# Performance work log

Hardware: AMD Instinct MI355X
Metric: run time of the kernel (lower is better)

The kernel has to match this reference:

```python
import jax, jax.numpy as jnp
import numpy as np


def setup_inputs() -> dict:
    key = jax.random.key(0)
    ks = jax.random.split(key, 11)
    B, S, D, K = 8, 2048, 512, 256
    s = lambda k, shp, fan: jax.random.normal(k, shp, dtype=jnp.float32) / np.sqrt(fan)
    return {
        "x": jax.random.normal(ks[0], (B, S, D), dtype=jnp.float32),
        "Wk1": s(ks[1], (D, K), D), "bk1": jnp.zeros((K,), jnp.float32),
        "Wq1": s(ks[2], (D, K), D), "bq1": jnp.zeros((K,), jnp.float32),
        "Wk2": s(ks[3], (D, K), D), "bk2": jnp.zeros((K,), jnp.float32),
        "Wq2": s(ks[4], (D, K), D), "bq2": jnp.zeros((K,), jnp.float32),
        "Wv2": s(ks[5], (D, D), D), "bv2": jnp.zeros((D,), jnp.float32),
    }


def _attn(q, k, v):
    # raw scores with NO 1/sqrt(d) scaling, softmax over key axis, then AV
    scores = jax.nn.softmax(jnp.einsum('bqd,bkd->bqk', q, k), axis=-1)
    return jnp.einsum('bqk,bkd->bqd', scores, v)


def _block2(h, Wk2, bk2, Wq2, bq2, Wv2, bv2):
    k = h @ Wk2 + bk2
    q = h @ Wq2 + bq2
    v = h @ Wv2 + bv2
    v = v / jnp.linalg.norm(v, axis=2, keepdims=True)  # L2-normalize values
    return _attn(q, k, v)


def reference(x, Wk1, bk1, Wq1, bq1, Wk2, bk2, Wq2, bq2, Wv2, bv2):
    # block 1: values are the raw input x
    k1 = x @ Wk1 + bk1
    q1 = x @ Wq1 + bq1
    outputs = _attn(q1, k1, x)
    # blocks 2 and 3 reuse the SAME layer-2 weights (as in the torch forward)
    hidden = _block2(outputs, Wk2, bk2, Wq2, bq2, Wv2, bv2)
    final = _block2(hidden, Wk2, bk2, Wq2, bq2, Wv2, bv2)
    return final[0, -1, :]
```

## Files before the change

### kernel.cpp

```cpp
#include <hip/hip_runtime.h>
#include <math.h>

typedef __attribute__((ext_vector_type(8))) short short8;
typedef __attribute__((ext_vector_type(4))) float f32x4;
typedef unsigned short us;

__device__ inline unsigned short f2bf_rn(float f) {
    unsigned u = __builtin_bit_cast(unsigned, f);
    u += 0x7FFF + ((u >> 16) & 1);
    return (unsigned short)(u >> 16);
}
__device__ inline float bf2f(unsigned short h) {
    unsigned u = ((unsigned)h) << 16;
    return __builtin_bit_cast(float, u);
}

#define ISSUE(ST, RA, RB)                                                      \
  do {                                                                         \
    int s_ = (ST);                                                             \
    int sg_ = s_ / SPS;                                                        \
    int k0_ = (s_ - sg_ * SPS) * 64;                                           \
    const unsigned short* Ap_ = (sg_ < 2) ? Ah : Al;                           \
    const unsigned short* Bp_ = (sg_ == 1) ? Bl : Bh;                          \
    _Pragma("unroll") for (int i_ = 0; i_ < 4; ++i_) {                         \
      RA[i_] = *(const uint4*)(Ap_ + (size_t)(bm + crow[i_]) * lda + k0_ + csl[i_] * 8); \
      RB[i_] = *(const uint4*)(Bp_ + (size_t)(bn + crow[i_]) * ldb + k0_ + csl[i_] * 8); \
    }                                                                          \
  } while (0)

#define PHASE(IT, RWa, RWb, RLa, RLb)                                          \
  do {                                                                         \
    _Pragma("unroll") for (int i_ = 0; i_ < 4; ++i_) {                         \
      int wsl_ = csl[i_] ^ (crow[i_] & 7);                                     \
      *(uint4*)&As[crow[i_]][wsl_ * 8] = RWa[i_];                              \
      *(uint4*)&Bs[crow[i_]][wsl_ * 8] = RWb[i_];                              \
    }                                                                          \
    if ((IT) + 1 < CHUNK) { ISSUE(st0 + (IT) + 1, RLa, RLb); }                 \
    asm volatile("s_waitcnt lgkmcnt(0)\n\ts_barrier" ::: "memory");            \
    _Pragma("unroll") for (int kk = 0; kk < 2; ++kk) {                         \
      short8 af[4], bf[4];                                                     \
      _Pragma("unroll") for (int f = 0; f < 4; ++f) {                          \
        int ar = wm * 64 + f * 16 + r15;                                       \
        int as_ = (kk * 4 + ksl) ^ (ar & 7);                                   \
        af[f] = *(const short8*)&As[ar][as_ * 8];                              \
        int br = wn * 64 + f * 16 + r15;                                       \
        int bs_ = (kk * 4 + ksl) ^ (br & 7);                                   \
        bf[f] = *(const short8*)&Bs[br][bs_ * 8];                              \
      }                                                                        \
      _Pragma("unroll") for (int i_ = 0; i_ < 4; ++i_)                         \
        _Pragma("unroll") for (int j_ = 0; j_ < 4; ++j_)                       \
          acc[i_][j_] = __builtin_amdgcn_mfma_f32_16x16x32_bf16(               \
              af[i_], bf[j_], acc[i_][j_], 0, 0, 0);                           \
    }                                                                          \
    asm volatile("s_barrier" ::: "memory");                                    \
  } while (0)

template <int KSEG, int NSPLIT>
__global__ __launch_bounds__(256, 2) void gemm_bf16(
    const unsigned short* __restrict__ Ah, const unsigned short* __restrict__ Al, int lda,
    const unsigned short* __restrict__ Bh, const unsigned short* __restrict__ Bl, int ldb,
    float* __restrict__ Cout, int ldc)
{
    constexpr int SPS = KSEG / 64;
    constexpr int NST = 3 * SPS;
    constexpr int CHUNK = NST / NSPLIT;

    __shared__ __align__(16) unsigned short As[128][64];
    __shared__ __align__(16) unsigned short Bs[128][64];

    const int tid = threadIdx.x, lane = tid & 63, w = tid >> 6;
    const int wm = w >> 1, wn = w & 1;
    const int bm = blockIdx.y * 128, bn = blockIdx.x * 128;
    const int st0 = blockIdx.z * CHUNK;
    const int r15 = lane & 15, ksl = lane >> 4;

    int crow[4], csl[4];
#pragma unroll
    for (int i = 0; i < 4; ++i) { int c = tid + i * 256; crow[i] = c >> 3; csl[i] = c & 7; }

    f32x4 acc[4][4];
#pragma unroll
    for (int i = 0; i < 4; ++i)
#pragma unroll
        for (int j = 0; j < 4; ++j) acc[i][j] = (f32x4){0.f, 0.f, 0.f, 0.f};

    uint4 rA0[4], rB0[4], rA1[4], rB1[4];
    ISSUE(st0, rA0, rB0);

#pragma unroll 1
    for (int it = 0; it < CHUNK; it += 2) {
        PHASE(it,     rA0, rB0, rA1, rB1);
        PHASE(it + 1, rA1, rB1, rA0, rB0);
    }

    float* Cz = Cout + (size_t)blockIdx.z * (size_t)(gridDim.y * 128) * ldc;
#pragma unroll
    for (int i = 0; i < 4; ++i) {
        int rowb = bm + wm * 64 + i * 16 + (lane >> 4) * 4;
#pragma unroll
        for (int j = 0; j < 4; ++j) {
            int colb = bn + wn * 64 + j * 16 + r15;
#pragma unroll
            for (int r = 0; r < 4; ++r)
                Cz[(size_t)(rowb + r) * ldc + colb] = acc[i][j][r];
        }
    }
}

template <int NS, bool BIAS, bool L2N>
__global__ __launch_bounds__(256) void reduce_kernel(
    const float* __restrict__ part, size_t pstride4,
    const float* __restrict__ bias, float* __restrict__ C,
    unsigned short* __restrict__ Ch, unsigned short* __restrict__ Cl, int N)
{
    __shared__ float red[4];
    const int tid = threadIdx.x;
    size_t idx = (size_t)blockIdx.x * 256 + tid;
    const float4* p = (const float4*)part;
    float4 s = p[idx];
#pragma unroll
    for (int z = 1; z < NS; ++z) {
        float4 t = p[idx + (size_t)z * pstride4];
        s.x += t.x; s.y += t.y; s.z += t.z; s.w += t.w;
    }
    if (BIAS) {
        int col = (int)((idx * 4) & (size_t)(N - 1));
        s.x += bias[col]; s.y += bias[col + 1]; s.z += bias[col + 2]; s.w += bias[col + 3];
    }
    if (L2N) {
        float ss = (tid >= 128) ? (s.x * s.x + s.y * s.y + s.z * s.z + s.w * s.w) : 0.f;
#pragma unroll
        for (int o = 32; o; o >>= 1) ss += __shfl_down(ss, o);
        if ((tid & 63) == 0) red[tid >> 6] = ss;
        __syncthreads();
        if (tid >= 128) {
            float scale = 1.f / sqrtf(red[2] + red[3]);
            s.x *= scale; s.y *= scale; s.z *= scale; s.w *= scale;
        }
    }
    ((float4*)C)[idx] = s;
    float v[4] = {s.x, s.y, s.z, s.w};
    unsigned short h[4], l[4];
#pragma unroll
    for (int q = 0; q < 4; ++q) { h[q] = f2bf_rn(v[q]); l[q] = f2bf_rn(v[q] - bf2f(h[q])); }
    uint2 hp = make_uint2((unsigned)h[0] | ((unsigned)h[1] << 16), (unsigned)h[2] | ((unsigned)h[3] << 16));
    uint2 lp = make_uint2((unsigned)l[0] | ((unsigned)l[1] << 16), (unsigned)l[2] | ((unsigned)l[3] << 16));
    ((uint2*)Ch)[idx] = hp;
    ((uint2*)Cl)[idx] = lp;
}

#define SLK(r, s) ((s) ^ (((s) >> 3) & 3) ^ ((((r) ^ ((r) >> 3))) & 7))

__global__ __launch_bounds__(256, 2) void flash_attn(
    const unsigned short* __restrict__ Qh, const unsigned short* __restrict__ Ql,
    const unsigned short* __restrict__ Kh, const unsigned short* __restrict__ Kl,
    int ldqk,
    const unsigned short* __restrict__ VTh, const unsigned short* __restrict__ VTl,
    float* __restrict__ Opart, float* __restrict__ Mpart, float* __restrict__ Lpart)
{
    const int tid = threadIdx.x, lane = tid & 63, w = tid >> 6;
    const int z = blockIdx.x;
    const int q0 = blockIdx.y * 64;
    const int dblk = blockIdx.z;
    const int s0 = z * 256;
    const int cc = lane & 15, g = lane >> 4;
    const int dbase = dblk * 256 + w * 64;

    __shared__ __align__(16) unsigned short KsH[32][256], KsL[32][256];
    __shared__ __align__(16) unsigned short PsH[64][32], PsL[64][32];
    __shared__ float Fs[64];
    __shared__ int flagAny[4];

    short8 qh[8], qlv[8];
#pragma unroll
    for (int ks = 0; ks < 8; ++ks) {
        const size_t qoff = (size_t)(q0 + w * 16 + cc) * ldqk + ks * 32 + g * 8;
        qh[ks]  = *(const short8*)(Qh + qoff);
        qlv[ks] = *(const short8*)(Ql + qoff);
    }

    f32x4 acc[4][4];
#pragma unroll
    for (int a = 0; a < 4; ++a)
#pragma unroll
        for (int b = 0; b < 4; ++b) acc[a][b] = (f32x4){0.f, 0.f, 0.f, 0.f};
    float m[4] = {-1e30f, -1e30f, -1e30f, -1e30f};
    float l[4] = {0.f, 0.f, 0.f, 0.f};

#pragma unroll 1
    for (int sub = 0; sub < 8; ++sub) {
        __syncthreads();
#pragma unroll
        for (int i = 0; i < 4; ++i) {
            int idx = tid + i * 256;
            int row = (idx >> 3) & 31;
            int sl  = (idx & 7) | ((idx >> 8) << 3);
            size_t go = (size_t)(s0 + sub * 32 + row) * ldqk + sl * 8;
            uint4 vh = *(const uint4*)(Kh + go);
            uint4 vl = *(const uint4*)(Kl + go);
            int sw = SLK(row, sl);
            *(uint4*)&KsH[row][sw * 8] = vh;
            *(uint4*)&KsL[row][sw * 8] = vl;
        }
        __syncthreads();

        f32x4 sac[2];
        sac[0] = (f32x4){0.f, 0.f, 0.f, 0.f};
        sac[1] = (f32x4){0.f, 0.f, 0.f, 0.f};
#pragma unroll
        for (int ks = 0; ks < 8; ++ks) {
#pragma unroll
            for (int t = 0; t < 2; ++t) {
                int row = t * 16 + cc;
                int sw = SLK(row, ks * 4 + g);
                short8 bh = *(const short8*)&KsH[row][sw * 8];
                short8 bl = *(const short8*)&KsL[row][sw * 8];
                sac[t] = __builtin_amdgcn_mfma_f32_16x16x32_bf16(qh[ks], bh, sac[t], 0, 0, 0);
                sac[t] = __builtin_amdgcn_mfma_f32_16x16x32_bf16(qh[ks], bl, sac[t], 0, 0, 0);
                sac[t] = __builtin_amdgcn_mfma_f32_16x16x32_bf16(qlv[ks], bh, sac[t], 0, 0, 0);
            }
        }

        float mt[4], fr[4];
        bool nb = false;
#pragma unroll
        for (int r = 0; r < 4; ++r) {
            float v = fmaxf(sac[0][r], sac[1][r]);
#pragma unroll
            for (int o = 8; o >= 1; o >>= 1) v = fmaxf(v, __shfl_xor(v, o));
            mt[r] = v;
            nb = nb || (v > m[r] + 8.f);
        }
        const int need = __any((int)nb);
        if (need) {
#pragma unroll
            for (int r = 0; r < 4; ++r) {
                float mn = fmaxf(m[r], mt[r]);
                fr[r] = __expf(m[r] - mn);
                m[r] = mn;
                l[r] *= fr[r];
            }
        } else {
#pragma unroll
            for (int r = 0; r < 4; ++r) fr[r] = 1.f;
        }
        if (cc == 0) {
#pragma unroll
            for (int r = 0; r < 4; ++r) Fs[w * 16 + g * 4 + r] = fr[r];
        }
        if (lane == 0) flagAny[w] = need;

#pragma unroll
        for (int t = 0; t < 2; ++t) {
            float ps[4];
#pragma unroll
            for (int r = 0; r < 4; ++r) {
                float pv = __expf(sac[t][r] - m[r]);
                ps[r] = pv;
                unsigned short ph = f2bf_rn(pv);
                unsigned short pl = f2bf_rn(pv - bf2f(ph));
                int qq = w * 16 + g * 4 + r;
                int kv = cc + 16 * t;
                int col = (((kv >> 3) ^ (qq & 3)) << 3) | (kv & 7);
                PsH[qq][col] = ph;
                PsL[qq][col] = pl;
            }
#pragma unroll
            for (int r = 0; r < 4; ++r) {
                float sv = ps[r];
#pragma unroll
                for (int o = 8; o >= 1; o >>= 1) sv += __shfl_xor(sv, o);
                l[r] += sv;
            }
        }
        __syncthreads();

        int anyf = flagAny[0] | flagAny[1] | flagAny[2] | flagAny[3];
        if (anyf) {
#pragma unroll
            for (int qt = 0; qt < 4; ++qt)
#pragma unroll
                for (int r = 0; r < 4; ++r) {
                    float fq = Fs[qt * 16 + g * 4 + r];
#pragma unroll
                    for (int dt = 0; dt < 4; ++dt) acc[qt][dt][r] *= fq;
                }
        }

        short8 pah[4], pal[4];
#pragma unroll
        for (int qt = 0; qt < 4; ++qt) {
            int qr = qt * 16 + cc;
            int col = (g ^ (qr & 3)) << 3;
            pah[qt] = *(const short8*)&PsH[qr][col];
            pal[qt] = *(const short8*)&PsL[qr][col];
        }
#pragma unroll
        for (int dt = 0; dt < 4; ++dt) {
            size_t vo = (size_t)(dbase + dt * 16 + cc) * 2048 + s0 + sub * 32 + g * 8;
            short8 vh = *(const short8*)(VTh + vo);
            short8 vl = *(const short8*)(VTl + vo);
#pragma unroll
            for (int qt = 0; qt < 4; ++qt) {
                acc[qt][dt] = __builtin_amdgcn_mfma_f32_16x16x32_bf16(pah[qt], vh, acc[qt][dt], 0, 0, 0);
                acc[qt][dt] = __builtin_amdgcn_mfma_f32_16x16x32_bf16(pah[qt], vl, acc[qt][dt], 0, 0, 0);
                acc[qt][dt] = __builtin_amdgcn_mfma_f32_16x16x32_bf16(pal[qt], vh, acc[qt][dt], 0, 0, 0);
            }
        }
    }

#pragma unroll
    for (int qt = 0; qt < 4; ++qt)
#pragma unroll
        for (int dt = 0; dt < 4; ++dt)
#pragma unroll
            for (int r = 0; r < 4; ++r) {
                int row = q0 + qt * 16 + g * 4 + r;
                int col = dbase + dt * 16 + cc;
                Opart[((size_t)z * 2048 + row) * 512 + col] = acc[qt][dt][r];
            }
    if (dblk == 0 && cc == 0) {
#pragma unroll
        for (int r = 0; r < 4; ++r) {
            int row = q0 + w * 16 + g * 4 + r;
            Mpart[z * 2048 + row] = m[r];
            Lpart[z * 2048 + row] = l[r];
        }
    }
}

__global__ __launch_bounds__(256) void flash_combine(
    const float* __restrict__ Opart, const float* __restrict__ Mpart,
    const float* __restrict__ Lpart,
    unsigned short* __restrict__ Oh, unsigned short* __restrict__ Ol)
{
    const int q = blockIdx.x;
    const int tid = threadIdx.x;
    float wz[8];
    float mstar = -1e30f;
#pragma unroll
    for (int zz = 0; zz < 8; ++zz) { wz[zz] = Mpart[zz * 2048 + q]; mstar = fmaxf(mstar, wz[zz]); }
    float L = 0.f;
#pragma unroll
    for (int zz = 0; zz < 8; ++zz) {
        float e = __expf(wz[zz] - mstar);
        L += e * Lpart[zz * 2048 + q];
        wz[zz] = e;
    }
    float invL = 1.f / L;
    int d = tid * 2;
    float sx = 0.f, sy = 0.f;
#pragma unroll
    for (int zz = 0; zz < 8; ++zz) {
        const float2 t = *(const float2*)(Opart + ((size_t)zz * 2048 + q) * 512 + d);
        sx += wz[zz] * t.x;
        sy += wz[zz] * t.y;
    }
    sx *= invL; sy *= invL;
    unsigned short h0 = f2bf_rn(sx), h1 = f2bf_rn(sy);
    unsigned short l0 = f2bf_rn(sx - bf2f(h0)), l1 = f2bf_rn(sy - bf2f(h1));
    *(unsigned*)(Oh + (size_t)q * 512 + d) = (unsigned)h0 | ((unsigned)h1 << 16);
    *(unsigned*)(Ol + (size_t)q * 512 + d) = (unsigned)l0 | ((unsigned)l1 << 16);
}

__global__ __launch_bounds__(256) void tc_kernel(
    const float* __restrict__ in, int ldin,
    unsigned short* __restrict__ oh, unsigned short* __restrict__ ol,
    int ldo, int rowoff)
{
    __shared__ float tile[32][33];
    int bx = blockIdx.x * 32, by = blockIdx.y * 32;
    int tx = threadIdx.x & 31, ty = threadIdx.x >> 5;
#pragma unroll
    for (int i = 0; i < 32; i += 8)
        tile[ty + i][tx] = in[(size_t)(by + ty + i) * ldin + bx + tx];
    __syncthreads();
#pragma unroll
    for (int i = 0; i < 32; i += 8) {
        float v = tile[tx][ty + i];
        unsigned short h = f2bf_rn(v);
        unsigned short l = f2bf_rn(v - bf2f(h));
        size_t o = (size_t)(rowoff + bx + ty + i) * ldo + by + tx;
        oh[o] = h; ol[o] = l;
    }
}

__global__ __launch_bounds__(256) void convert_hl(
    const float* __restrict__ in, unsigned short* __restrict__ oh,
    unsigned short* __restrict__ ol)
{
    size_t idx = (size_t)blockIdx.x * 256 + threadIdx.x;
    float4 s = ((const float4*)in)[idx];
    float v[4] = {s.x, s.y, s.z, s.w};
    unsigned short h[4], l[4];
#pragma unroll
    for (int q = 0; q < 4; ++q) { h[q] = f2bf_rn(v[q]); l[q] = f2bf_rn(v[q] - bf2f(h[q])); }
    uint2 hp = make_uint2((unsigned)h[0] | ((unsigned)h[1] << 16), (unsigned)h[2] | ((unsigned)h[3] << 16));
    uint2 lp = make_uint2((unsigned)l[0] | ((unsigned)l[1] << 16), (unsigned)l[2] | ((unsigned)l[3] << 16));
    ((uint2*)oh)[idx] = hp;
    ((uint2*)ol)[idx] = lp;
}

__global__ __launch_bounds__(256) void concat_bias(
    const float* bk1, const float* bq1, const float* bk2, const float* bq2,
    const float* bv2, float* b1, float* b2)
{
    int i = blockIdx.x * 256 + threadIdx.x;
    if (i < 512) b1[i] = (i < 256) ? bk1[i] : bq1[i - 256];
    if (i < 1024) b2[i] = (i < 256) ? bk2[i] : (i < 512 ? bq2[i - 256] : bv2[i - 512]);
}

template <bool HAS_BIAS>
__global__ __launch_bounds__(256) void gemv_nt(
    const float* __restrict__ a, const float* __restrict__ Bt, int ldb,
    const float* __restrict__ bias, float* __restrict__ out, int K)
{
    int w = threadIdx.x >> 6, lane = threadIdx.x & 63;
    int n = blockIdx.x * 4 + w;
    const float* row = Bt + (size_t)n * ldb;
    float s = 0.f;
    for (int k = lane; k < K; k += 64) s = fmaf(a[k], row[k], s);
#pragma unroll
    for (int o = 32; o; o >>= 1) s += __shfl_down(s, o);
    if (lane == 0) out[n] = HAS_BIAS ? s + bias[n] : s;
}

__global__ __launch_bounds__(256) void gemv_hl(
    const float* __restrict__ p, const unsigned short* __restrict__ Vh,
    const unsigned short* __restrict__ Vl, int ld, float* __restrict__ out, int K)
{
    int w = threadIdx.x >> 6, lane = threadIdx.x & 63;
    int d = blockIdx.x * 4 + w;
    const unsigned short* rh = Vh + (size_t)d * ld;
    const unsigned short* rl = Vl + (size_t)d * ld;
    float s = 0.f;
    for (int k = lane; k < K; k += 64) s = fmaf(p[k], bf2f(rh[k]) + bf2f(rl[k]), s);
#pragma unroll
    for (int o = 32; o; o >>= 1) s += __shfl_down(s, o);
    if (lane == 0) out[d] = s;
}

__global__ __launch_bounds__(256) void softmax_f32(float* __restrict__ S, int L)
{
    __shared__ float row[2048];
    __shared__ float red[8];
    const int tid = threadIdx.x;
    float* p = S + (size_t)blockIdx.x * L;
    float mx = -1e30f;
    for (int i = tid; i < L; i += 256) { float v = p[i]; row[i] = v; mx = fmaxf(mx, v); }
#pragma unroll
    for (int o = 32; o; o >>= 1) mx = fmaxf(mx, __shfl_down(mx, o));
    if ((tid & 63) == 0) red[tid >> 6] = mx;
    __syncthreads();
    mx = fmaxf(fmaxf(red[0], red[1]), fmaxf(red[2], red[3]));
    float sum = 0.f;
    for (int i = tid; i < L; i += 256) { float e = expf(row[i] - mx); row[i] = e; sum += e; }
#pragma unroll
    for (int o = 32; o; o >>= 1) sum += __shfl_down(sum, o);
    __syncthreads();
    if ((tid & 63) == 0) red[4 + (tid >> 6)] = sum;
    __syncthreads();
    float inv = 1.f / (red[4] + red[5] + red[6] + red[7]);
    for (int i = tid; i < L; i += 256) p[i] = row[i] * inv;
}

extern "C" void kernel_launch(void* const* d_in, const int* in_sizes, int n_in,
                              void* d_out, int out_size, void* d_ws, size_t ws_size,
                              hipStream_t stream)
{
    const float* x   = (const float*)d_in[0];
    const float* Wk1 = (const float*)d_in[1];
    const float* bk1 = (const float*)d_in[2];
    const float* Wq1 = (const float*)d_in[3];
    const float* bq1 = (const float*)d_in[4];
    const float* Wk2 = (const float*)d_in[5];
    const float* bk2 = (const float*)d_in[6];
    const float* Wq2 = (const float*)d_in[7];
    const float* bq2 = (const float*)d_in[8];
    const float* Wv2 = (const float*)d_in[9];
    const float* bv2 = (const float*)d_in[10];
    float* out = (float*)d_out;

    const int S = 2048, D = 512;

    char* p = (char*)d_ws;
    float* C   = (float*)p;  p += (size_t)S * 1024 * 4;
    float* BIG = (float*)p;  p += (size_t)8 * S * 512 * 4;
    float* Mp  = (float*)p;  p += (size_t)8 * S * 4;
    float* Lp  = (float*)p;  p += (size_t)8 * S * 4;
    us* Chh = (us*)p; p += (size_t)S * 1024 * 2;
    us* Cll = (us*)p; p += (size_t)S * 1024 * 2;
    us* Hh  = (us*)p; p += (size_t)S * D * 2;
    us* Hl  = (us*)p; p += (size_t)S * D * 2;
    us* xh  = (us*)p; p += (size_t)S * D * 2;
    us* xl  = (us*)p; p += (size_t)S * D * 2;
    us* VTh = (us*)p; p += (size_t)D * S * 2;
    us* VTl = (us*)p; p += (size_t)D * S * 2;
    us* WT1h = (us*)p; p += (size_t)512 * 512 * 2;
    us* WT1l = (us*)p; p += (size_t)512 * 512 * 2;
    us* WT2h = (us*)p; p += (size_t)1024 * 512 * 2;
    us* WT2l = (us*)p; p += (size_t)1024 * 512 * 2;
    float* b1 = (float*)p; p += 512 * 4;
    float* b2 = (float*)p; p += 1024 * 4;

    dim3 blk(256);
    const size_t PSTR  = (size_t)S * 512 / 4;
    const size_t PSTR2 = (size_t)S * 1024 / 4;

    convert_hl<<<dim3(S * D / 1024), blk, 0, stream>>>(x, xh, xl);
    tc_kernel<<<dim3(16, 64), blk, 0, stream>>>(x, 512, VTh, VTl, S, 0);
    tc_kernel<<<dim3(8, 16), blk, 0, stream>>>(Wk1, 256, WT1h, WT1l, 512, 0);
    tc_kernel<<<dim3(8, 16), blk, 0, stream>>>(Wq1, 256, WT1h, WT1l, 512, 256);
    tc_kernel<<<dim3(8, 16), blk, 0, stream>>>(Wk2, 256, WT2h, WT2l, 512, 0);
    tc_kernel<<<dim3(8, 16), blk, 0, stream>>>(Wq2, 256, WT2h, WT2l, 512, 256);
    tc_kernel<<<dim3(16, 16), blk, 0, stream>>>(Wv2, 512, WT2h, WT2l, 512, 512);
    concat_bias<<<dim3(4), blk, 0, stream>>>(bk1, bq1, bk2, bq2, bv2, b1, b2);

    gemm_bf16<512, 6><<<dim3(4, 16, 6), blk, 0, stream>>>(xh, xl, 512, WT1h, WT1l, 512, BIG, 512);
    reduce_kernel<6, true, false><<<dim3(S * 512 / 1024), blk, 0, stream>>>(BIG, PSTR, b1, C, Chh, Cll, 512);
    flash_attn<<<dim3(8, 32, 2), blk, 0, stream>>>(Chh + 256, Cll + 256, Chh, Cll, 512,
                                                   VTh, VTl, BIG, Mp, Lp);
    flash_combine<<<dim3(S), blk, 0, stream>>>(BIG, Mp, Lp, Hh, Hl);

    gemm_bf16<512, 4><<<dim3(8, 16, 4), blk, 0, stream>>>(Hh, Hl, 512, WT2h, WT2l, 512, BIG, 1024);
    reduce_kernel<4, true, true><<<dim3(S * 1024 / 1024), blk, 0, stream>>>(BIG, PSTR2, b2, C, Chh, Cll, 1024);
    tc_kernel<<<dim3(16, 64), blk, 0, stream>>>(C + 512, 1024, VTh, VTl, S, 0);
    flash_attn<<<dim3(8, 32, 2), blk, 0, stream>>>(Chh + 256, Cll + 256, Chh, Cll, 1024,
                                                   VTh, VTl, BIG, Mp, Lp);
    flash_combine<<<dim3(S), blk, 0, stream>>>(BIG, Mp, Lp, Hh, Hl);

    gemm_bf16<512, 4><<<dim3(8, 16, 4), blk, 0, stream>>>(Hh, Hl, 512, WT2h, WT2l, 512, BIG, 1024);
    reduce_kernel<4, true, true><<<dim3(S * 1024 / 1024), blk, 0, stream>>>(BIG, PSTR2, b2, C, Chh, Cll, 1024);
    tc_kernel<<<dim3(16, 64), blk, 0, stream>>>(C + 512, 1024, VTh, VTl, S, 0);
    gemv_nt<false><<<dim3(S / 4), blk, 0, stream>>>(C + (size_t)(S - 1) * 1024 + 256, C, 1024,
                                                    nullptr, BIG, 256);
    softmax_f32<<<dim3(1), blk, 0, stream>>>(BIG, S);
    gemv_hl<<<dim3(D / 4), blk, 0, stream>>>(BIG, VTh, VTl, S, out, S);
}
```

Before: 389.5 us.

## Prefetch K tiles and V fragments in flash_attn; merge setup kernels

In flash_attn, the K tile for the next sub-block is loaded into registers while the current one is written to shared memory, and the V fragments are issued before the score computation. This hides global load latency behind MFMA work and drops one barrier per iteration. Separately, the eight small setup launches (conversion, transposes, bias concat) are merged into two kernels to cut launch overhead. The trade-off is higher register pressure from the prefetch buffers, which could reduce occupancy at launch_bounds(256,2).

After: 520.5 us. 1.34x slower.

```diff
diff --git a/kernel.cpp b/kernel.cpp
--- a/kernel.cpp
+++ b/kernel.cpp
@@ -64,6 +64,7 @@
     constexpr int SPS = KSEG / 64;
     constexpr int NST = 3 * SPS;
     constexpr int CHUNK = NST / NSPLIT;
+    static_assert((CHUNK & 1) == 0, "CHUNK must be even");
 
     __shared__ __align__(16) unsigned short As[128][64];
     __shared__ __align__(16) unsigned short Bs[128][64];
@@ -150,6 +151,16 @@
 }
 
 #define SLK(r, s) ((s) ^ (((s) >> 3) & 3) ^ ((((r) ^ ((r) >> 3))) & 7))
+
+#define KISSUE(SUB)                                                            \
+  do {                                                                         \
+    int ns_ = (SUB) & 7;                                                       \
+    _Pragma("unroll") for (int i_ = 0; i_ < 4; ++i_) {                         \
+      size_t go_ = (size_t)(s0 + ns_ * 32 + srow[i_]) * ldqk + ssl[i_] * 8;    \
+      krh[i_] = *(const uint4*)(Kh + go_);                                     \
+      krl[i_] = *(const uint4*)(Kl + go_);                                     \
+    }                                                                          \
+  } while (0)
 
 __global__ __launch_bounds__(256, 2) void flash_attn(
     const unsigned short* __restrict__ Qh, const unsigned short* __restrict__ Ql,
@@ -171,6 +182,15 @@
     __shared__ float Fs[64];
     __shared__ int flagAny[4];
 
+    int srow[4], ssl[4], ssw[4];
+#pragma unroll
+    for (int i = 0; i < 4; ++i) {
+        int idx = tid + i * 256;
+        srow[i] = (idx >> 3) & 31;
+        ssl[i]  = (idx & 7) | ((idx >> 8) << 3);
+        ssw[i]  = SLK(srow[i], ssl[i]);
+    }
+
     short8 qh[8], qlv[8];
 #pragma unroll
     for (int ks = 0; ks < 8; ++ks) {
@@ -187,20 +207,24 @@
     float m[4] = {-1e30f, -1e30f, -1e30f, -1e30f};
     float l[4] = {0.f, 0.f, 0.f, 0.f};
 
+    uint4 krh[4], krl[4];
+    KISSUE(0);
+
 #pragma unroll 1
     for (int sub = 0; sub < 8; ++sub) {
-        __syncthreads();
 #pragma unroll
         for (int i = 0; i < 4; ++i) {
-            int idx = tid + i * 256;
-            int row = (idx >> 3) & 31;
-            int sl  = (idx & 7) | ((idx >> 8) << 3);
-            size_t go = (size_t)(s0 + sub * 32 + row) * ldqk + sl * 8;
-            uint4 vh = *(const uint4*)(Kh + go);
-            uint4 vl = *(const uint4*)(Kl + go);
-            int sw = SLK(row, sl);
-            *(uint4*)&KsH[row][sw * 8] = vh;
-            *(uint4*)&KsL[row][sw * 8] = vl;
+            *(uint4*)&KsH[srow[i]][ssw[i] * 8] = krh[i];
+            *(uint4*)&KsL[srow[i]][ssw[i] * 8] = krl[i];
+        }
+        KISSUE(sub + 1);
+
+        uint4 vph[4], vpl[4];
+#pragma unroll
+        for (int dt = 0; dt < 4; ++dt) {
+            size_t vo = (size_t)(dbase + dt * 16 + cc) * 2048 + s0 + sub * 32 + g * 8;
+            vph[dt] = *(const uint4*)(VTh + vo);
+            vpl[dt] = *(const uint4*)(VTl + vo);
         }
         __syncthreads();
 
@@ -297,9 +321,8 @@
         }
 #pragma unroll
         for (int dt = 0; dt < 4; ++dt) {
-            size_t vo = (size_t)(dbase + dt * 16 + cc) * 2048 + s0 + sub * 32 + g * 8;
-            short8 vh = *(const short8*)(VTh + vo);
-            short8 vl = *(const short8*)(VTl + vo);
+            short8 vh = __builtin_bit_cast(short8, vph[dt]);
+            short8 vl = __builtin_bit_cast(short8, vpl[dt]);
 #pragma unroll
             for (int qt = 0; qt < 4; ++qt) {
                 acc[qt][dt] = __builtin_amdgcn_mfma_f32_16x16x32_bf16(pah[qt], vh, acc[qt][dt], 0, 0, 0);
@@ -363,13 +386,12 @@
     *(unsigned*)(Ol + (size_t)q * 512 + d) = (unsigned)l0 | ((unsigned)l1 << 16);
 }
 
-__global__ __launch_bounds__(256) void tc_kernel(
-    const float* __restrict__ in, int ldin,
-    unsigned short* __restrict__ oh, unsigned short* __restrict__ ol,
-    int ldo, int rowoff)
+__device__ inline void tc_dev(const float* __restrict__ in, int ldin,
+                              unsigned short* __restrict__ oh, unsigned short* __restrict__ ol,
+                              int ldo, int rowoff, int bxt, int byt)
 {
     __shared__ float tile[32][33];
-    int bx = blockIdx.x * 32, by = blockIdx.y * 32;
+    int bx = bxt * 32, by = byt * 32;
     int tx = threadIdx.x & 31, ty = threadIdx.x >> 5;
 #pragma unroll
     for (int i = 0; i < 32; i += 8)
@@ -385,29 +407,67 @@
     }
 }
 
-__global__ __launch_bounds__(256) void convert_hl(
-    const float* __restrict__ in, unsigned short* __restrict__ oh,
-    unsigned short* __restrict__ ol)
-{
-    size_t idx = (size_t)blockIdx.x * 256 + threadIdx.x;
-    float4 s = ((const float4*)in)[idx];
-    float v[4] = {s.x, s.y, s.z, s.w};
-    unsigned short h[4], l[4];
-#pragma unroll
-    for (int q = 0; q < 4; ++q) { h[q] = f2bf_rn(v[q]); l[q] = f2bf_rn(v[q] - bf2f(h[q])); }
-    uint2 hp = make_uint2((unsigned)h[0] | ((unsigned)h[1] << 16), (unsigned)h[2] | ((unsigned)h[3] << 16));
-    uint2 lp = make_uint2((unsigned)l[0] | ((unsigned)l[1] << 16), (unsigned)l[2] | ((unsigned)l[3] << 16));
-    ((uint2*)oh)[idx] = hp;
-    ((uint2*)ol)[idx] = lp;
-}
-
-__global__ __launch_bounds__(256) void concat_bias(
-    const float* bk1, const float* bq1, const float* bk2, const float* bq2,
-    const float* bv2, float* b1, float* b2)
-{
-    int i = blockIdx.x * 256 + threadIdx.x;
-    if (i < 512) b1[i] = (i < 256) ? bk1[i] : bq1[i - 256];
-    if (i < 1024) b2[i] = (i < 256) ? bk2[i] : (i < 512 ? bq2[i - 256] : bv2[i - 512]);
+__global__ __launch_bounds__(256) void tc_kernel(
+    const float* __restrict__ in, int ldin,
+    unsigned short* __restrict__ oh, unsigned short* __restrict__ ol,
+    int ldo, int rowoff)
+{
+    tc_dev(in, ldin, oh, ol, ldo, rowoff, blockIdx.x, blockIdx.y);
+}
+
+__global__ __launch_bounds__(256) void setup_w(
+    const float* __restrict__ Wk1, const float* __restrict__ Wq1,
+    const float* __restrict__ Wk2, const float* __restrict__ Wq2,
+    const float* __restrict__ Wv2,
+    const float* __restrict__ bk1, const float* __restrict__ bq1,
+    const float* __restrict__ bk2, const float* __restrict__ bq2,
+    const float* __restrict__ bv2,
+    unsigned short* __restrict__ WT1h, unsigned short* __restrict__ WT1l,
+    unsigned short* __restrict__ WT2h, unsigned short* __restrict__ WT2l,
+    float* __restrict__ b1, float* __restrict__ b2)
+{
+    int bid = blockIdx.x;
+    if (bid < 512) {
+        int which = bid >> 7;
+        int local = bid & 127;
+        const float* in; unsigned short *oh, *ol; int rowoff;
+        if (which == 0)      { in = Wk1; oh = WT1h; ol = WT1l; rowoff = 0; }
+        else if (which == 1) { in = Wq1; oh = WT1h; ol = WT1l; rowoff = 256; }
+        else if (which == 2) { in = Wk2; oh = WT2h; ol = WT2l; rowoff = 0; }
+        else                 { in = Wq2; oh = WT2h; ol = WT2l; rowoff = 256; }
+        tc_dev(in, 256, oh, ol, 512, rowoff, local & 7, local >> 3);
+    } else if (bid < 768) {
+        int local = bid - 512;
+        tc_dev(Wv2, 512, WT2h, WT2l, 512, 512, local & 15, local >> 4);
+    } else {
+        for (int i = threadIdx.x; i < 1024; i += 256) {
+            if (i < 512) b1[i] = (i < 256) ? bk1[i] : bq1[i - 256];
+            b2[i] = (i < 256) ? bk2[i] : (i < 512 ? bq2[i - 256] : bv2[i - 512]);
+        }
+    }
+}
+
+__global__ __launch_bounds__(256) void setup_x(
+    const float* __restrict__ x,
+    unsigned short* __restrict__ xh, unsigned short* __restrict__ xl,
+    unsigned short* __restrict__ vth, unsigned short* __restrict__ vtl)
+{
+    int bid = blockIdx.x;
+    if (bid < 1024) {
+        size_t idx = (size_t)bid * 256 + threadIdx.x;
+        float4 s = ((const float4*)x)[idx];
+        float v[4] = {s.x, s.y, s.z, s.w};
+        unsigned short h[4], l[4];
+#pragma unroll
+        for (int q = 0; q < 4; ++q) { h[q] = f2bf_rn(v[q]); l[q] = f2bf_rn(v[q] - bf2f(h[q])); }
+        uint2 hp = make_uint2((unsigned)h[0] | ((unsigned)h[1] << 16), (unsigned)h[2] | ((unsigned)h[3] << 16));
+        uint2 lp = make_uint2((unsigned)l[0] | ((unsigned)l[1] << 16), (unsigned)l[2] | ((unsigned)l[3] << 16));
+        ((uint2*)xh)[idx] = hp;
+        ((uint2*)xl)[idx] = lp;
+    } else {
+        int local = bid - 1024;
+        tc_dev(x, 512, vth, vtl, 2048, 0, local & 15, local >> 4);
+    }
 }
 
 template <bool HAS_BIAS>
@@ -507,14 +567,10 @@
     const size_t PSTR  = (size_t)S * 512 / 4;
     const size_t PSTR2 = (size_t)S * 1024 / 4;
 
-    convert_hl<<<dim3(S * D / 1024), blk, 0, stream>>>(x, xh, xl);
-    tc_kernel<<<dim3(16, 64), blk, 0, stream>>>(x, 512, VTh, VTl, S, 0);
-    tc_kernel<<<dim3(8, 16), blk, 0, stream>>>(Wk1, 256, WT1h, WT1l, 512, 0);
-    tc_kernel<<<dim3(8, 16), blk, 0, stream>>>(Wq1, 256, WT1h, WT1l, 512, 256);
-    tc_kernel<<<dim3(8, 16), blk, 0, stream>>>(Wk2, 256, WT2h, WT2l, 512, 0);
-    tc_kernel<<<dim3(8, 16), blk, 0, stream>>>(Wq2, 256, WT2h, WT2l, 512, 256);
-    tc_kernel<<<dim3(16, 16), blk, 0, stream>>>(Wv2, 512, WT2h, WT2l, 512, 512);
-    concat_bias<<<dim3(4), blk, 0, stream>>>(bk1, bq1, bk2, bq2, bv2, b1, b2);
+    setup_x<<<dim3(2048), blk, 0, stream>>>(x, xh, xl, VTh, VTl);
+    setup_w<<<dim3(769), blk, 0, stream>>>(Wk1, Wq1, Wk2, Wq2, Wv2,
+                                           bk1, bq1, bk2, bq2, bv2,
+                                           WT1h, WT1l, WT2h, WT2l, b1, b2);
 
     gemm_bf16<512, 6><<<dim3(4, 16, 6), blk, 0, stream>>>(xh, xl, 512, WT1h, WT1l, 512, BIG, 512);
     reduce_kernel<6, true, false><<<dim3(S * 512 / 1024), blk, 0, stream>>>(BIG, PSTR, b1, C, Chh, Cll, 512);
```
